# Optimization experiments

Hardware: AMD Instinct MI355X
Metric: run time of the kernel (lower is better)

## Reference

```python
import jax, jax.numpy as jnp
import numpy as np

BETA = 1.0
POWER_ITERS = 9
EPS = 1e-12  # F.normalize default eps


def _normalize(v):
    # L2 normalize over dim=1 of [B, N, 1], matching F.normalize(x, dim=1)
    n = jnp.linalg.norm(v, axis=1, keepdims=True)
    return v / jnp.maximum(n, EPS)


def _dominant_eigenvalue(A, x):
    # A: [B, N, N], x: [B, N, 1]
    for _ in range(POWER_ITERS):
        x = _normalize(jnp.matmul(A, x))
    Ax = jnp.matmul(A, x)[..., 0]              # [B, N]
    num = jnp.sum(Ax * x[..., 0], axis=1)      # x^T A x
    den = jnp.sum(x[..., 0] ** 2, axis=1)      # ||x||^2 (== 1 after normalize)
    return num / den, x


def setup_inputs() -> dict:
    key = jax.random.key(0)
    k1, k2 = jax.random.split(key)
    B, C, H, W = 256, 2048, 7, 7
    x = jax.random.normal(k1, (B, C, H, W), dtype=jnp.float32)
    x0 = _normalize(jax.random.normal(k2, (B, H * W, 1), dtype=jnp.float32))
    return {"x": x, "x0": x0}


def reference(x, x0):
    B, C, H, W = x.shape
    N = H * W
    Wm = x.reshape(B, C, N)
    # ATA = W^T W : [B, N, N]
    ATA = jnp.einsum('bcn,bcm->bnm', Wm, Wm)
    # first power iteration: largest eigenvalue; x0 is a no_grad constant
    largest, x1 = _dominant_eigenvalue(ATA, jax.lax.stop_gradient(x0))
    I = jnp.eye(N, dtype=ATA.dtype)
    shifted = ATA - largest[:, None, None] * I
    # second power iteration warm-started from detached x1 (torch stores last_x detached)
    tmp, _ = _dominant_eigenvalue(shifted, jax.lax.stop_gradient(x1))
    smallest = tmp + largest
    penalty = BETA * (largest / smallest - 1.0) ** 2
    return jnp.sum(penalty) / B
```

## Files before the change

kernel.cpp:

```cpp
#include <hip/hip_runtime.h>
#include <hip/hip_bf16.h>
#include <stdint.h>


#define BATCH 256
#define CDIM  2048
#define NDIM  49
#define CHUNK 64
#define NCHUNK (CDIM / CHUNK)
#define ITEMS (NDIM * (CHUNK / 8))
#define CHUNK_FLOATS (CHUNK * NDIM)

typedef __bf16 bf16x8 __attribute__((ext_vector_type(8)));
typedef float  f32x16 __attribute__((ext_vector_type(16)));
typedef float  f32x4  __attribute__((ext_vector_type(4)));

union V16 {
  f32x4  f4;
  bf16x8 b8;
};

__device__ __forceinline__ void load8(const float* __restrict__ g,
                                      float (&r)[8]) {
#pragma unroll
  for (int j = 0; j < 8; ++j) r[j] = g[j * NDIM];
}

__device__ __forceinline__ void cvt_store(const float (&r)[8], uint32_t* Hb,
                                          uint32_t* Lb, int w) {
  bf16x8 hv, lv;
#pragma unroll
  for (int j = 0; j < 8; ++j) {
    float e = r[j];
    __bf16 h = (__bf16)e;
    hv[j] = h;
    lv[j] = (__bf16)(e - (float)h);
  }
  V16 a, b;
  a.b8 = hv;
  b.b8 = lv;
  *(f32x4*)(Hb + w) = a.f4;
  *(f32x4*)(Lb + w) = b.f4;
}

__device__ __forceinline__ void comp16(const uint32_t* Hb, const uint32_t* Lb,
                                       int m, int n, int hf, f32x16& c1,
                                       f32x16& c2, f32x16& c3) {
  const f32x4* H = (const f32x4*)Hb;
  const f32x4* L = (const f32x4*)Lb;
#pragma unroll
  for (int s = 0; s < 4; ++s) {
    const int blk = 2 * s + hf;
    V16 ah, al, bh, bl;
    ah.f4 = H[m * 8 + (blk ^ (m & 7))];
    al.f4 = L[m * 8 + (blk ^ (m & 7))];
    bh.f4 = H[n * 8 + (blk ^ (n & 7))];
    bl.f4 = L[n * 8 + (blk ^ (n & 7))];
    c1 = __builtin_amdgcn_mfma_f32_32x32x16_bf16(ah.b8, bh.b8, c1, 0, 0, 0);
    c2 = __builtin_amdgcn_mfma_f32_32x32x16_bf16(ah.b8, bl.b8, c2, 0, 0, 0);
    c3 = __builtin_amdgcn_mfma_f32_32x32x16_bf16(al.b8, bh.b8, c3, 0, 0, 0);
  }
}

__global__ __launch_bounds__(256) void fused_kernel(
    const float* __restrict__ x, const float* __restrict__ x0,
    float* __restrict__ pen) {
  __shared__ __align__(16) uint32_t ldsHi[2][2048];
  __shared__ __align__(16) uint32_t ldsLo[2][2048];
  __shared__ __align__(16) float A[NDIM * NDIM + 3];

  const int tid  = threadIdx.x;
  const int b    = blockIdx.x;
  const int lane = tid & 63;
  const int wv   = tid >> 6;
  const int ln   = lane & 31;
  const int hf   = lane >> 5;
  const int qm = wv >> 1, qn = wv & 1;
  const int m = qm * 32 + ln;
  const int n = qn * 32 + ln;

  const float* gbase = x + (size_t)b * (CDIM * NDIM);

  const int i0 = tid;
  const int i1 = tid + 256;
  const bool v1 = (i1 < ITEMS);
  const int kq0 = (i0 * 1338) >> 16;
  const int n0  = i0 - 49 * kq0;
  const int kq1 = (i1 * 1338) >> 16;
  const int n1  = i1 - 49 * kq1;
  const int g0  = kq0 * (8 * NDIM) + n0;
  const int g1  = kq1 * (8 * NDIM) + n1;
  const int w0  = n0 * 32 + 4 * (kq0 ^ (n0 & 7));
  const int w1  = n1 * 32 + 4 * (kq1 ^ (n1 & 7));

  f32x16 c1, c2, c3;
#pragma unroll
  for (int i = 0; i < 16; ++i) { c1[i] = 0.f; c2[i] = 0.f; c3[i] = 0.f; }

  float sA0[8], sA1[8], sB0[8], sB1[8];

  load8(gbase + g0, sA0);
  if (v1) load8(gbase + g1, sA1);

  for (int ch = 0; ch < NCHUNK; ch += 2) {
    {
      const float* gch = gbase + (size_t)(ch + 1) * CHUNK_FLOATS;
      load8(gch + g0, sB0);
      if (v1) load8(gch + g1, sB1);
    }
    cvt_store(sA0, ldsHi[0], ldsLo[0], w0);
    if (v1) cvt_store(sA1, ldsHi[0], ldsLo[0], w1);
    __syncthreads();
    comp16(ldsHi[0], ldsLo[0], m, n, hf, c1, c2, c3);

    if (ch + 2 < NCHUNK) {
      const float* gch = gbase + (size_t)(ch + 2) * CHUNK_FLOATS;
      load8(gch + g0, sA0);
      if (v1) load8(gch + g1, sA1);
    }
    cvt_store(sB0, ldsHi[1], ldsLo[1], w0);
    if (v1) cvt_store(sB1, ldsHi[1], ldsLo[1], w1);
    __syncthreads();
    comp16(ldsHi[1], ldsLo[1], m, n, hf, c1, c2, c3);
  }

#pragma unroll
  for (int r = 0; r < 16; ++r) {
    int row = (r & 3) + 8 * (r >> 2) + 4 * hf;
    int mm = qm * 32 + row;
    if (mm < NDIM && n < NDIM)
      A[mm * NDIM + n] = c1[r] + c2[r] + c3[r];
  }
  __syncthreads();

  if (tid < 64) {
    const bool act = (tid < NDIM);
    float Ar[NDIM];
    {
      const float* Arow = &A[(act ? tid : (NDIM - 1)) * NDIM];
#pragma unroll
      for (int k = 0; k < NDIM; ++k) Ar[k] = Arow[k];
    }
    float xl = act ? x0[b * NDIM + tid] : 0.f;

    auto rayleigh = [&](float shift) -> float {
      for (int it = 0; it < 9; ++it) {
        float a0 = 0.f, a1 = 0.f, a2 = 0.f, a3 = 0.f;
#pragma unroll
        for (int k = 0; k < 48; k += 4) {
          a0 = fmaf(Ar[k + 0], __shfl(xl, k + 0, 64), a0);
          a1 = fmaf(Ar[k + 1], __shfl(xl, k + 1, 64), a1);
          a2 = fmaf(Ar[k + 2], __shfl(xl, k + 2, 64), a2);
          a3 = fmaf(Ar[k + 3], __shfl(xl, k + 3, 64), a3);
        }
        a0 = fmaf(Ar[48], __shfl(xl, 48, 64), a0);
        float y = act ? (((a0 + a1) + (a2 + a3)) - shift * xl) : 0.f;
        float s2 = y * y;
#pragma unroll
        for (int o = 32; o; o >>= 1) s2 += __shfl_xor(s2, o, 64);
        xl = y / fmaxf(sqrtf(s2), 1e-12f);
      }
      float a0 = 0.f, a1 = 0.f, a2 = 0.f, a3 = 0.f;
#pragma unroll
      for (int k = 0; k < 48; k += 4) {
        a0 = fmaf(Ar[k + 0], __shfl(xl, k + 0, 64), a0);
        a1 = fmaf(Ar[k + 1], __shfl(xl, k + 1, 64), a1);
        a2 = fmaf(Ar[k + 2], __shfl(xl, k + 2, 64), a2);
        a3 = fmaf(Ar[k + 3], __shfl(xl, k + 3, 64), a3);
      }
      a0 = fmaf(Ar[48], __shfl(xl, 48, 64), a0);
      float yy = act ? (((a0 + a1) + (a2 + a3)) - shift * xl) : 0.f;
      float num = yy * xl;
      float den = xl * xl;
#pragma unroll
      for (int o = 32; o; o >>= 1) {
        num += __shfl_xor(num, o, 64);
        den += __shfl_xor(den, o, 64);
      }
      return num / den;
    };

    float largest  = rayleigh(0.f);
    float smallest = rayleigh(largest) + largest;
    if (tid == 0) {
      float r = largest / smallest - 1.f;
      pen[b] = r * r;
    }
  }
}

__global__ __launch_bounds__(64) void finish_kernel(
    const float* __restrict__ pen, float* __restrict__ out) {
  const int t = threadIdx.x;
  float s = pen[t] + pen[t + 64] + pen[t + 128] + pen[t + 192];
#pragma unroll
  for (int o = 32; o; o >>= 1) s += __shfl_xor(s, o, 64);
  if (t == 0) out[0] = s * (1.0f / (float)BATCH);
}

extern "C" void kernel_launch(void* const* d_in, const int* in_sizes, int n_in,
                              void* d_out, int out_size, void* d_ws,
                              size_t ws_size, hipStream_t stream) {
  const float* x  = (const float*)d_in[0];
  const float* x0 = (const float*)d_in[1];
  float* out = (float*)d_out;
  float* pen = (float*)d_ws;

  fused_kernel<<<BATCH, 256, 0, stream>>>(x, x0, pen);
  finish_kernel<<<1, 64, 0, stream>>>(pen, out);
}
```

Baseline: 172.8 us.

## Split channel reduction across four wave groups per block with LDS combine

Each block now runs 1024 threads split into four groups of 256. Each group accumulates the Gram matrix over a quarter of the channel dimension using its own double-buffered LDS region. The partial results are then summed into shared memory one group at a time, separated by barriers. This puts more waves on each batch item to shorten the serial K loop and hide memory latency. The cost is more LDS per block (128KB), block-wide barriers inside the loop that now stall all 16 waves, and a serialized reduction step.

```diff
diff --git a/kernel.cpp b/kernel.cpp
--- a/kernel.cpp
+++ b/kernel.cpp
@@ -6,8 +6,10 @@
 #define BATCH 256
 #define CDIM  2048
 #define NDIM  49
+#define GROUPS 4
+#define GK    (CDIM / GROUPS)
 #define CHUNK 64
-#define NCHUNK (CDIM / CHUNK)
+#define NCHUNK (GK / CHUNK)
 #define ITEMS (NDIM * (CHUNK / 8))
 #define CHUNK_FLOATS (CHUNK * NDIM)
 
@@ -26,8 +28,8 @@
   for (int j = 0; j < 8; ++j) r[j] = g[j * NDIM];
 }
 
-__device__ __forceinline__ void cvt_store(const float (&r)[8], uint32_t* Hb,
-                                          uint32_t* Lb, int w) {
+__device__ __forceinline__ void cvt_store(const float (&r)[8], float* Hb,
+                                          float* Lb, int w) {
   bf16x8 hv, lv;
 #pragma unroll
   for (int j = 0; j < 8; ++j) {
@@ -43,7 +45,7 @@
   *(f32x4*)(Lb + w) = b.f4;
 }
 
-__device__ __forceinline__ void comp16(const uint32_t* Hb, const uint32_t* Lb,
+__device__ __forceinline__ void comp16(const float* Hb, const float* Lb,
                                        int m, int n, int hf, f32x16& c1,
                                        f32x16& c2, f32x16& c3) {
   const f32x4* H = (const f32x4*)Hb;
@@ -62,27 +64,31 @@
   }
 }
 
-__global__ __launch_bounds__(256) void fused_kernel(
+__global__ __launch_bounds__(1024) void fused_kernel(
     const float* __restrict__ x, const float* __restrict__ x0,
     float* __restrict__ pen) {
-  __shared__ __align__(16) uint32_t ldsHi[2][2048];
-  __shared__ __align__(16) uint32_t ldsLo[2][2048];
-  __shared__ __align__(16) float A[NDIM * NDIM + 3];
+  __shared__ __align__(16) float lds[32768];
 
   const int tid  = threadIdx.x;
   const int b    = blockIdx.x;
+  const int g    = tid >> 8;
+  const int ltid = tid & 255;
   const int lane = tid & 63;
-  const int wv   = tid >> 6;
+  const int gw   = (tid >> 6) & 3;
   const int ln   = lane & 31;
   const int hf   = lane >> 5;
-  const int qm = wv >> 1, qn = wv & 1;
+  const int qm = gw >> 1, qn = gw & 1;
   const int m = qm * 32 + ln;
   const int n = qn * 32 + ln;
 
-  const float* gbase = x + (size_t)b * (CDIM * NDIM);
-
-  const int i0 = tid;
-  const int i1 = tid + 256;
+  float* const buf0 = lds + g * 8192;
+  float* const buf1 = lds + g * 8192 + 4096;
+
+  const float* gbase = x + (size_t)b * (CDIM * NDIM)
+                         + (size_t)g * (GK * NDIM);
+
+  const int i0 = ltid;
+  const int i1 = ltid + 256;
   const bool v1 = (i1 < ITEMS);
   const int kq0 = (i0 * 1338) >> 16;
   const int n0  = i0 - 49 * kq0;
@@ -102,36 +108,47 @@
   load8(gbase + g0, sA0);
   if (v1) load8(gbase + g1, sA1);
 
+#pragma unroll
   for (int ch = 0; ch < NCHUNK; ch += 2) {
     {
       const float* gch = gbase + (size_t)(ch + 1) * CHUNK_FLOATS;
       load8(gch + g0, sB0);
       if (v1) load8(gch + g1, sB1);
     }
-    cvt_store(sA0, ldsHi[0], ldsLo[0], w0);
-    if (v1) cvt_store(sA1, ldsHi[0], ldsLo[0], w1);
+    cvt_store(sA0, buf0, buf0 + 2048, w0);
+    if (v1) cvt_store(sA1, buf0, buf0 + 2048, w1);
     __syncthreads();
-    comp16(ldsHi[0], ldsLo[0], m, n, hf, c1, c2, c3);
+    comp16(buf0, buf0 + 2048, m, n, hf, c1, c2, c3);
 
     if (ch + 2 < NCHUNK) {
       const float* gch = gbase + (size_t)(ch + 2) * CHUNK_FLOATS;
       load8(gch + g0, sA0);
       if (v1) load8(gch + g1, sA1);
     }
-    cvt_store(sB0, ldsHi[1], ldsLo[1], w0);
-    if (v1) cvt_store(sB1, ldsHi[1], ldsLo[1], w1);
+    cvt_store(sB0, buf1, buf1 + 2048, w0);
+    if (v1) cvt_store(sB1, buf1, buf1 + 2048, w1);
     __syncthreads();
-    comp16(ldsHi[1], ldsLo[1], m, n, hf, c1, c2, c3);
-  }
-
-#pragma unroll
-  for (int r = 0; r < 16; ++r) {
-    int row = (r & 3) + 8 * (r >> 2) + 4 * hf;
-    int mm = qm * 32 + row;
-    if (mm < NDIM && n < NDIM)
-      A[mm * NDIM + n] = c1[r] + c2[r] + c3[r];
-  }
+    comp16(buf1, buf1 + 2048, m, n, hf, c1, c2, c3);
+  }
+
+  float* A = lds;
   __syncthreads();
+#pragma unroll
+  for (int gg = 0; gg < GROUPS; ++gg) {
+    if (g == gg) {
+#pragma unroll
+      for (int r = 0; r < 16; ++r) {
+        int row = (r & 3) + 8 * (r >> 2) + 4 * hf;
+        int mm = qm * 32 + row;
+        if (mm < NDIM && n < NDIM) {
+          float v = c1[r] + c2[r] + c3[r];
+          if (gg == 0) A[mm * NDIM + n] = v;
+          else         A[mm * NDIM + n] += v;
+        }
+      }
+    }
+    __syncthreads();
+  }
 
   if (tid < 64) {
     const bool act = (tid < NDIM);
@@ -206,6 +223,6 @@
   float* out = (float*)d_out;
   float* pen = (float*)d_ws;
 
-  fused_kernel<<<BATCH, 256, 0, stream>>>(x, x0, pen);
+  fused_kernel<<<BATCH, 1024, 0, stream>>>(x, x0, pen);
   finish_kernel<<<1, 64, 0, stream>>>(pen, out);
 }
```

Result: faster. 168.3 us (-2.6%).
